# Kernel optimization log

Hardware: AMD Instinct MI355X
Metric: run time of the kernel (lower is better)

Reference implementation:

```python
import jax, jax.numpy as jnp
import numpy as np

B, C, L = 4, 256, 4096
H = 8
DK = C // H


def setup_inputs() -> dict:
    key = jax.random.key(0)
    kx, kq, kk, kv, kl = jax.random.split(key, 5)
    scale = 1.0 / np.sqrt(C)
    return {
        "x": jax.random.normal(kx, (B, C, L), dtype=jnp.float32),
        "Wq": jax.random.normal(kq, (C, C), dtype=jnp.float32) * scale,
        "Wk": jax.random.normal(kk, (C, C), dtype=jnp.float32) * scale,
        "Wv": jax.random.normal(kv, (C, C), dtype=jnp.float32) * scale,
        "Wl": jax.random.normal(kl, (C, C), dtype=jnp.float32) * scale,
    }


def reference(x, Wq, Wk, Wv, Wl):
    # Conv1d with kernel_size=1, no bias == channel-mixing matmul per position.
    def proj(W, t):  # W: [C_out, C_in], t: [B, C_in, L] -> [B, L, H, DK]
        y = jnp.einsum('oc,bcl->blo', W, t)
        return y.reshape(B, L, H, DK)

    q = proj(Wq, x)  # [B, L, H, DK]
    k = proj(Wk, x)
    v = proj(Wv, x)

    # scores: [B, H, L, L]
    scores = jnp.einsum('bqhd,bkhd->bhqk', q, k) / jnp.sqrt(jnp.float32(DK))
    p_attn = jax.nn.softmax(scores, axis=-1)
    # attention output with post-ReLU: [B, L, H, DK] -> [B, L, C]
    out = jax.nn.relu(jnp.einsum('bhqk,bkhd->bqhd', p_attn, v)).reshape(B, L, C)
    # last_conv: [B, C_out, L]
    return jnp.einsum('oc,blc->bol', Wl, out)
```

## Files before the change

### kernel.cpp

```cpp
#include <hip/hip_runtime.h>

#define L_DIM 4096
#define C_DIM 256
#define B_DIM 4
#define NH 8
#define DK 32

#define QSCALE 0.25507694f

typedef __bf16 bf16x8 __attribute__((ext_vector_type(8)));
typedef float  f32x4  __attribute__((ext_vector_type(4)));
typedef float  f32x16 __attribute__((ext_vector_type(16)));

static __device__ __forceinline__ unsigned pk_bf16(float lo, float hi) {
    unsigned a = __builtin_bit_cast(unsigned, lo) + 0x8000u;
    unsigned b = __builtin_bit_cast(unsigned, hi) + 0x8000u;
    return __builtin_amdgcn_perm(b, a, 0x07060302u);
}

__global__ __launch_bounds__(256) void transpose_x_kernel(
    const float* __restrict__ x, __bf16* __restrict__ xt)
{
    const int t  = threadIdx.x;
    const int l0 = blockIdx.x * 64;
    const int c0 = blockIdx.y * 64;
    const int b  = blockIdx.z;

    __shared__ __attribute__((aligned(16))) float T[64][65];

    {
        const int r  = t >> 2;
        const int lc = (t & 3) * 16;
        const float* xp = x + ((size_t)b * C_DIM + c0 + r) * L_DIM + l0 + lc;
        #pragma unroll
        for (int k = 0; k < 4; ++k)
            *(f32x4*)&T[r][lc + k * 4] = *(const f32x4*)(xp + k * 4);
    }
    __syncthreads();
    {
        const int l  = t >> 2;
        const int cc = (t & 3) * 16;
        unsigned u[8];
        #pragma unroll
        for (int i = 0; i < 8; ++i)
            u[i] = pk_bf16(T[cc + 2 * i][l], T[cc + 2 * i + 1][l]);
        __bf16* op = xt + ((size_t)b * L_DIM + l0 + l) * C_DIM + c0 + cc;
        *(uint4*)op       = make_uint4(u[0], u[1], u[2], u[3]);
        *(uint4*)(op + 8) = make_uint4(u[4], u[5], u[6], u[7]);
    }
}

__global__ __launch_bounds__(256) void proj_mfma_kernel(
    const __bf16* __restrict__ xt, const float* __restrict__ Wq,
    const float* __restrict__ Wk, const float* __restrict__ Wv,
    __bf16* __restrict__ Qb, __bf16* __restrict__ Kb, __bf16* __restrict__ Vb)
{
    const int t    = threadIdx.x;
    const int wave = t >> 6;
    const int lane = t & 63;
    const int n32  = lane & 31;
    const int hl   = lane >> 5;
    const int l0   = blockIdx.x * 128;
    const int ob   = blockIdx.y & 1;
    const int p    = blockIdx.y >> 1;
    const int b    = blockIdx.z;
    const float* W = (p == 0) ? Wq : ((p == 1) ? Wk : Wv);
    const float sc = (p == 0) ? QSCALE : 1.0f;

    __shared__ __attribute__((aligned(16))) __bf16 Wt[128][72];
    __shared__ __attribute__((aligned(16))) __bf16 Xs[128][72];

    const int wo  = t >> 1, wcc = (t & 1) * 32;
    const int xl  = t >> 1, xcc = (t & 1) * 32;
    const float*  wg = W + (size_t)(ob * 128 + wo) * C_DIM + wcc;
    const __bf16* xg = xt + ((size_t)b * L_DIM + l0 + xl) * C_DIM + xcc;

    const int moff = (wave & 1) * 64;
    const int noff = (wave >> 1) * 64;

    f32x16 acc[2][2];
    #pragma unroll
    for (int i = 0; i < 2; ++i)
        #pragma unroll
        for (int j = 0; j < 2; ++j)
            #pragma unroll
            for (int r = 0; r < 16; ++r) acc[i][j][r] = 0.f;

    unsigned wpk[16];
    bf16x8   xpr[4];
    #pragma unroll
    for (int k = 0; k < 8; ++k) {
        f32x4 wv = *(const f32x4*)(wg + k * 4);
        wpk[k * 2]     = pk_bf16(wv[0] * sc, wv[1] * sc);
        wpk[k * 2 + 1] = pk_bf16(wv[2] * sc, wv[3] * sc);
    }
    #pragma unroll
    for (int g = 0; g < 4; ++g) xpr[g] = *(const bf16x8*)(xg + g * 8);

    for (int bk = 0; bk < 4; ++bk) {
        __syncthreads();
        #pragma unroll
        for (int g = 0; g < 4; ++g) {
            *(uint4*)&Wt[wo][wcc + g * 8] =
                make_uint4(wpk[g*4], wpk[g*4+1], wpk[g*4+2], wpk[g*4+3]);
            *(bf16x8*)&Xs[xl][xcc + g * 8] = xpr[g];
        }
        if (bk < 3) {
            #pragma unroll
            for (int k = 0; k < 8; ++k) {
                f32x4 wv = *(const f32x4*)(wg + (bk + 1) * 64 + k * 4);
                wpk[k * 2]     = pk_bf16(wv[0] * sc, wv[1] * sc);
                wpk[k * 2 + 1] = pk_bf16(wv[2] * sc, wv[3] * sc);
            }
            #pragma unroll
            for (int g = 0; g < 4; ++g)
                xpr[g] = *(const bf16x8*)(xg + (bk + 1) * 64 + g * 8);
        }
        __syncthreads();

        #pragma unroll
        for (int ks = 0; ks < 4; ++ks) {
            bf16x8 a0 = *(const bf16x8*)&Wt[moff + n32     ][ks * 16 + hl * 8];
            bf16x8 a1 = *(const bf16x8*)&Wt[moff + 32 + n32][ks * 16 + hl * 8];
            bf16x8 b0 = *(const bf16x8*)&Xs[noff + n32     ][ks * 16 + hl * 8];
            bf16x8 b1 = *(const bf16x8*)&Xs[noff + 32 + n32][ks * 16 + hl * 8];
            acc[0][0] = __builtin_amdgcn_mfma_f32_32x32x16_bf16(a0, b0, acc[0][0], 0, 0, 0);
            acc[0][1] = __builtin_amdgcn_mfma_f32_32x32x16_bf16(a0, b1, acc[0][1], 0, 0, 0);
            acc[1][0] = __builtin_amdgcn_mfma_f32_32x32x16_bf16(a1, b0, acc[1][0], 0, 0, 0);
            acc[1][1] = __builtin_amdgcn_mfma_f32_32x32x16_bf16(a1, b1, acc[1][1], 0, 0, 0);
        }
    }

    #pragma unroll
    for (int mt = 0; mt < 2; ++mt) {
        const int o32 = ob * 128 + moff + mt * 32;
        const int h   = o32 >> 5;
        const int bh  = b * NH + h;
        #pragma unroll
        for (int nt = 0; nt < 2; ++nt) {
            const int l = l0 + noff + nt * 32 + n32;
            if (p < 2) {
                __bf16* out = ((p == 0) ? Qb : Kb) + ((size_t)bh * L_DIM + l) * DK;
                #pragma unroll
                for (int g = 0; g < 4; ++g) {
                    unsigned u0 = pk_bf16(acc[mt][nt][g*4],     acc[mt][nt][g*4+1]);
                    unsigned u1 = pk_bf16(acc[mt][nt][g*4+2],   acc[mt][nt][g*4+3]);
                    *(uint2*)(out + 4 * hl + 8 * g) = make_uint2(u0, u1);
                }
            } else {
                #pragma unroll
                for (int r = 0; r < 16; ++r) {
                    const int dk = (r & 3) + 4 * hl + 8 * (r >> 2);
                    Vb[((size_t)bh * DK + dk) * L_DIM + l] = (__bf16)acc[mt][nt][r];
                }
            }
        }
    }
}

__global__ __launch_bounds__(256) void attn_kernel(
    const __bf16* __restrict__ Q, const __bf16* __restrict__ K,
    const __bf16* __restrict__ V, __bf16* __restrict__ Op0,
    __bf16* __restrict__ Op1, float* __restrict__ Ls)
{
    const int tid   = threadIdx.x;
    const int wave  = tid >> 6;
    const int lane  = tid & 63;
    const int n32   = lane & 31;
    const int hl    = lane >> 5;
    const int h     = blockIdx.y;
    const int b     = blockIdx.z >> 1;
    const int khalf = blockIdx.z & 1;
    const int bh    = b * NH + h;
    const int q0    = blockIdx.x * 256 + wave * 64;
    const int kt0   = khalf * 32;

    __shared__ __attribute__((aligned(16))) __bf16 Ks[64][40];
    __shared__ __attribute__((aligned(16))) __bf16 Vs[32][72];

    bf16x8 qf[2][2];
    #pragma unroll
    for (int qt = 0; qt < 2; ++qt) {
        const __bf16* qp = Q + ((size_t)bh * L_DIM + q0 + qt * 32 + n32) * DK;
        qf[qt][0] = *(const bf16x8*)(qp + hl * 8);
        qf[qt][1] = *(const bf16x8*)(qp + 16 + hl * 8);
    }

    f32x16 oacc[2], lacc[2];
    #pragma unroll
    for (int qt = 0; qt < 2; ++qt)
        #pragma unroll
        for (int r = 0; r < 16; ++r) { oacc[qt][r] = 0.f; lacc[qt][r] = 0.f; }

    const f32x16 z16 = {};

    bf16x8 ones;
    #pragma unroll
    for (int j = 0; j < 8; ++j) ones[j] = (__bf16)1.0f;

    const __bf16* kg = K + (size_t)bh * L_DIM * DK + (tid >> 2) * DK + (tid & 3) * 8;
    const __bf16* vg = V + ((size_t)bh * DK + (tid >> 3)) * L_DIM + (tid & 7) * 8;
    __bf16* ksd = &Ks[tid >> 2][(tid & 3) * 8];
    const int va  = tid & 7;
    __bf16* vsd0 = &Vs[tid >> 3][(va >> 1) * 16 + (va & 1) * 4];
    __bf16* vsd1 = vsd0 + 8;

    bf16x8 kreg = *(const bf16x8*)(kg + (size_t)kt0 * 64 * DK);
    bf16x8 vreg = *(const bf16x8*)(vg + kt0 * 64);

    for (int kt = 0; kt < 32; ++kt) {
        __syncthreads();
        *(bf16x8*)ksd = kreg;
        union { bf16x8 v; uint2 u2[2]; } vv; vv.v = vreg;
        *(uint2*)vsd0 = vv.u2[0];
        *(uint2*)vsd1 = vv.u2[1];
        {
            const int nkt = kt0 + ((kt + 1) & 31);
            kreg = *(const bf16x8*)(kg + (size_t)nkt * 64 * DK);
            vreg = *(const bf16x8*)(vg + nkt * 64);
        }
        __syncthreads();

        bf16x8 kf[2][2];
        kf[0][0] = *(const bf16x8*)&Ks[n32     ][hl * 8];
        kf[0][1] = *(const bf16x8*)&Ks[n32     ][16 + hl * 8];
        kf[1][0] = *(const bf16x8*)&Ks[32 + n32][hl * 8];
        kf[1][1] = *(const bf16x8*)&Ks[32 + n32][16 + hl * 8];
        bf16x8 vf[4];
        vf[0] = *(const bf16x8*)&Vs[n32][     hl * 8];
        vf[1] = *(const bf16x8*)&Vs[n32][16 + hl * 8];
        vf[2] = *(const bf16x8*)&Vs[n32][32 + hl * 8];
        vf[3] = *(const bf16x8*)&Vs[n32][48 + hl * 8];

        #pragma unroll
        for (int mt = 0; mt < 2; ++mt) {
            #pragma unroll
            for (int qt = 0; qt < 2; ++qt) {
                f32x16 s = __builtin_amdgcn_mfma_f32_32x32x16_bf16(
                    kf[mt][0], qf[qt][0], z16, 0, 0, 0);
                s = __builtin_amdgcn_mfma_f32_32x32x16_bf16(
                    kf[mt][1], qf[qt][1], s, 0, 0, 0);

                float e[16];
                #pragma unroll
                for (int r = 0; r < 16; ++r) e[r] = __builtin_amdgcn_exp2f(s[r]);
                union { unsigned u[4]; bf16x8 v; } p0, p1;
                #pragma unroll
                for (int i = 0; i < 4; ++i) {
                    p0.u[i] = pk_bf16(e[2 * i],     e[2 * i + 1]);
                    p1.u[i] = pk_bf16(e[8 + 2 * i], e[8 + 2 * i + 1]);
                }

                oacc[qt] = __builtin_amdgcn_mfma_f32_32x32x16_bf16(
                    vf[mt * 2],     p0.v, oacc[qt], 0, 0, 0);
                lacc[qt] = __builtin_amdgcn_mfma_f32_32x32x16_bf16(
                    ones,           p0.v, lacc[qt], 0, 0, 0);
                oacc[qt] = __builtin_amdgcn_mfma_f32_32x32x16_bf16(
                    vf[mt * 2 + 1], p1.v, oacc[qt], 0, 0, 0);
                lacc[qt] = __builtin_amdgcn_mfma_f32_32x32x16_bf16(
                    ones,           p1.v, lacc[qt], 0, 0, 0);
            }
        }
    }

    __bf16* Op = khalf ? Op1 : Op0;
    #pragma unroll
    for (int qt = 0; qt < 2; ++qt) {
        const int l = q0 + qt * 32 + n32;
        __bf16* ap = Op + ((size_t)b * L_DIM + l) * C_DIM + h * 32 + 4 * hl;
        #pragma unroll
        for (int g = 0; g < 4; ++g) {
            *(uint2*)(ap + 8 * g) = make_uint2(
                pk_bf16(oacc[qt][g*4],     oacc[qt][g*4+1]),
                pk_bf16(oacc[qt][g*4+2],   oacc[qt][g*4+3]));
        }
        Ls[((size_t)khalf * B_DIM * NH + bh) * L_DIM + l] = lacc[qt][0];
    }
}

__global__ __launch_bounds__(256) void final_mfma_kernel(
    const __bf16* __restrict__ Op0, const __bf16* __restrict__ Op1,
    const float* __restrict__ Ls, const float* __restrict__ Wl,
    float* __restrict__ y)
{
    const int t    = threadIdx.x;
    const int wave = t >> 6;
    const int lane = t & 63;
    const int n32  = lane & 31;
    const int hl   = lane >> 5;
    const int l0   = blockIdx.x * 64;
    const int ob   = blockIdx.y;
    const int b    = blockIdx.z;

    __shared__ __attribute__((aligned(16))) __bf16 Wt[128][72];
    __shared__ __attribute__((aligned(16))) __bf16 Xs[64][72];

    const int wo  = t >> 1, wcc = (t & 1) * 32;
    const int xl  = t >> 2, xcc = (t & 3) * 16;
    const float* wg = Wl + (size_t)(ob * 128 + wo) * C_DIM + wcc;
    const size_t obase = ((size_t)b * L_DIM + l0 + xl) * C_DIM + xcc;

    float inv[4];
    {
        const int lidx = l0 + xl;
        #pragma unroll
        for (int bk = 0; bk < 4; ++bk) {
            const int hh = (bk * 64 + xcc) >> 5;
            const float l1 = Ls[((size_t)0 * B_DIM * NH + b * NH + hh) * L_DIM + lidx];
            const float l2 = Ls[((size_t)1 * B_DIM * NH + b * NH + hh) * L_DIM + lidx];
            inv[bk] = __builtin_amdgcn_rcpf(l1 + l2);
        }
    }

    const int moff = (wave & 1) * 64;
    const int noff = (wave >> 1) * 32;

    f32x16 acc[2];
    #pragma unroll
    for (int i = 0; i < 2; ++i)
        #pragma unroll
        for (int r = 0; r < 16; ++r) acc[i][r] = 0.f;

    unsigned wpk[16];
    bf16x8   o1r, o2r;
    #pragma unroll
    for (int k = 0; k < 8; ++k) {
        f32x4 wv = *(const f32x4*)(wg + k * 4);
        wpk[k * 2]     = pk_bf16(wv[0], wv[1]);
        wpk[k * 2 + 1] = pk_bf16(wv[2], wv[3]);
    }
    o1r = *(const bf16x8*)(Op0 + obase);
    o2r = *(const bf16x8*)(Op1 + obase);
    bf16x8 o1r2 = *(const bf16x8*)(Op0 + obase + 8);
    bf16x8 o2r2 = *(const bf16x8*)(Op1 + obase + 8);

    for (int bk = 0; bk < 4; ++bk) {
        __syncthreads();
        #pragma unroll
        for (int g = 0; g < 4; ++g)
            *(uint4*)&Wt[wo][wcc + g * 8] =
                make_uint4(wpk[g*4], wpk[g*4+1], wpk[g*4+2], wpk[g*4+3]);
        {
            unsigned u[4];
            #pragma unroll
            for (int i = 0; i < 4; ++i) {
                float v0 = ((float)o1r[2*i]   + (float)o2r[2*i]  ) * inv[bk];
                float v1 = ((float)o1r[2*i+1] + (float)o2r[2*i+1]) * inv[bk];
                v0 = v0 > 0.f ? v0 : 0.f;
                v1 = v1 > 0.f ? v1 : 0.f;
                u[i] = pk_bf16(v0, v1);
            }
            *(uint4*)&Xs[xl][xcc] = make_uint4(u[0], u[1], u[2], u[3]);
            #pragma unroll
            for (int i = 0; i < 4; ++i) {
                float v0 = ((float)o1r2[2*i]   + (float)o2r2[2*i]  ) * inv[bk];
                float v1 = ((float)o1r2[2*i+1] + (float)o2r2[2*i+1]) * inv[bk];
                v0 = v0 > 0.f ? v0 : 0.f;
                v1 = v1 > 0.f ? v1 : 0.f;
                u[i] = pk_bf16(v0, v1);
            }
            *(uint4*)&Xs[xl][xcc + 8] = make_uint4(u[0], u[1], u[2], u[3]);
        }
        if (bk < 3) {
            #pragma unroll
            for (int k = 0; k < 8; ++k) {
                f32x4 wv = *(const f32x4*)(wg + (bk + 1) * 64 + k * 4);
                wpk[k * 2]     = pk_bf16(wv[0], wv[1]);
                wpk[k * 2 + 1] = pk_bf16(wv[2], wv[3]);
            }
            o1r  = *(const bf16x8*)(Op0 + obase + (bk + 1) * 64);
            o2r  = *(const bf16x8*)(Op1 + obase + (bk + 1) * 64);
            o1r2 = *(const bf16x8*)(Op0 + obase + (bk + 1) * 64 + 8);
            o2r2 = *(const bf16x8*)(Op1 + obase + (bk + 1) * 64 + 8);
        }
        __syncthreads();

        #pragma unroll
        for (int ks = 0; ks < 4; ++ks) {
            bf16x8 a0 = *(const bf16x8*)&Wt[moff + n32     ][ks * 16 + hl * 8];
            bf16x8 a1 = *(const bf16x8*)&Wt[moff + 32 + n32][ks * 16 + hl * 8];
            bf16x8 b0 = *(const bf16x8*)&Xs[noff + n32     ][ks * 16 + hl * 8];
            acc[0] = __builtin_amdgcn_mfma_f32_32x32x16_bf16(a0, b0, acc[0], 0, 0, 0);
            acc[1] = __builtin_amdgcn_mfma_f32_32x32x16_bf16(a1, b0, acc[1], 0, 0, 0);
        }
    }

    #pragma unroll
    for (int mt = 0; mt < 2; ++mt) {
        #pragma unroll
        for (int r = 0; r < 16; ++r) {
            const int o = ob * 128 + moff + mt * 32 + (r & 3) + 4 * hl + 8 * (r >> 2);
            y[((size_t)b * C_DIM + o) * L_DIM + l0 + noff + n32] = acc[mt][r];
        }
    }
}

extern "C" void kernel_launch(void* const* d_in, const int* in_sizes, int n_in,
                              void* d_out, int out_size, void* d_ws, size_t ws_size,
                              hipStream_t stream)
{
    const float* x  = (const float*)d_in[0];
    const float* Wq = (const float*)d_in[1];
    const float* Wk = (const float*)d_in[2];
    const float* Wv = (const float*)d_in[3];
    const float* Wl = (const float*)d_in[4];
    float* y = (float*)d_out;

    const size_t n = (size_t)B_DIM * NH * L_DIM * DK;
    __bf16* Qb  = (__bf16*)d_ws;
    __bf16* Kb  = Qb + n;
    __bf16* Vb  = Kb + n;
    __bf16* Xt  = Vb + n;
    __bf16* Op0 = Xt;
    __bf16* Op1 = Xt + n;
    float*  Ls  = (float*)(Op1 + n);

    transpose_x_kernel<<<dim3(L_DIM/64, C_DIM/64, B_DIM), 256, 0, stream>>>(x, Xt);
    proj_mfma_kernel<<<dim3(L_DIM/128, 6, B_DIM), 256, 0, stream>>>(
        Xt, Wq, Wk, Wv, Qb, Kb, Vb);
    attn_kernel<<<dim3(L_DIM/256, NH, B_DIM * 2), 256, 0, stream>>>(
        Qb, Kb, Vb, Op0, Op1, Ls);
    final_mfma_kernel<<<dim3(L_DIM/64, 2, B_DIM), 256, 0, stream>>>(
        Op0, Op1, Ls, Wl, y);
}
```

Baseline: 216.3 us.

## Overlap global prefetch with MFMA compute and compute softmax denominator on VALU

```diff
diff --git a/kernel.cpp b/kernel.cpp
--- a/kernel.cpp
+++ b/kernel.cpp
@@ -86,14 +86,10 @@
             #pragma unroll
             for (int r = 0; r < 16; ++r) acc[i][j][r] = 0.f;
 
-    unsigned wpk[16];
-    bf16x8   xpr[4];
-    #pragma unroll
-    for (int k = 0; k < 8; ++k) {
-        f32x4 wv = *(const f32x4*)(wg + k * 4);
-        wpk[k * 2]     = pk_bf16(wv[0] * sc, wv[1] * sc);
-        wpk[k * 2 + 1] = pk_bf16(wv[2] * sc, wv[3] * sc);
-    }
+    f32x4  wraw[8];
+    bf16x8 xpr[4];
+    #pragma unroll
+    for (int k = 0; k < 8; ++k) wraw[k] = *(const f32x4*)(wg + k * 4);
     #pragma unroll
     for (int g = 0; g < 4; ++g) xpr[g] = *(const bf16x8*)(xg + g * 8);
 
@@ -101,22 +97,24 @@
         __syncthreads();
         #pragma unroll
         for (int g = 0; g < 4; ++g) {
-            *(uint4*)&Wt[wo][wcc + g * 8] =
-                make_uint4(wpk[g*4], wpk[g*4+1], wpk[g*4+2], wpk[g*4+3]);
+            unsigned u0 = pk_bf16(wraw[g*2][0] * sc, wraw[g*2][1] * sc);
+            unsigned u1 = pk_bf16(wraw[g*2][2] * sc, wraw[g*2][3] * sc);
+            unsigned u2 = pk_bf16(wraw[g*2+1][0] * sc, wraw[g*2+1][1] * sc);
+            unsigned u3 = pk_bf16(wraw[g*2+1][2] * sc, wraw[g*2+1][3] * sc);
+            *(uint4*)&Wt[wo][wcc + g * 8] = make_uint4(u0, u1, u2, u3);
             *(bf16x8*)&Xs[xl][xcc + g * 8] = xpr[g];
         }
-        if (bk < 3) {
-            #pragma unroll
-            for (int k = 0; k < 8; ++k) {
-                f32x4 wv = *(const f32x4*)(wg + (bk + 1) * 64 + k * 4);
-                wpk[k * 2]     = pk_bf16(wv[0] * sc, wv[1] * sc);
-                wpk[k * 2 + 1] = pk_bf16(wv[2] * sc, wv[3] * sc);
-            }
+        __syncthreads();
+
+        {
+            const int nbk = (bk + 1) & 3;
+            #pragma unroll
+            for (int k = 0; k < 8; ++k)
+                wraw[k] = *(const f32x4*)(wg + nbk * 64 + k * 4);
             #pragma unroll
             for (int g = 0; g < 4; ++g)
-                xpr[g] = *(const bf16x8*)(xg + (bk + 1) * 64 + g * 8);
-        }
-        __syncthreads();
+                xpr[g] = *(const bf16x8*)(xg + nbk * 64 + g * 8);
+        }
 
         #pragma unroll
         for (int ks = 0; ks < 4; ++ks) {
@@ -186,17 +184,14 @@
         qf[qt][1] = *(const bf16x8*)(qp + 16 + hl * 8);
     }
 
-    f32x16 oacc[2], lacc[2];
+    f32x16 oacc[2];
+    float  lsum[2] = {0.f, 0.f};
     #pragma unroll
     for (int qt = 0; qt < 2; ++qt)
         #pragma unroll
-        for (int r = 0; r < 16; ++r) { oacc[qt][r] = 0.f; lacc[qt][r] = 0.f; }
+        for (int r = 0; r < 16; ++r) oacc[qt][r] = 0.f;
 
     const f32x16 z16 = {};
-
-    bf16x8 ones;
-    #pragma unroll
-    for (int j = 0; j < 8; ++j) ones[j] = (__bf16)1.0f;
 
     const __bf16* kg = K + (size_t)bh * L_DIM * DK + (tid >> 2) * DK + (tid & 3) * 8;
     const __bf16* vg = V + ((size_t)bh * DK + (tid >> 3)) * L_DIM + (tid & 7) * 8;
@@ -214,12 +209,13 @@
         union { bf16x8 v; uint2 u2[2]; } vv; vv.v = vreg;
         *(uint2*)vsd0 = vv.u2[0];
         *(uint2*)vsd1 = vv.u2[1];
+        __syncthreads();
+
         {
             const int nkt = kt0 + ((kt + 1) & 31);
             kreg = *(const bf16x8*)(kg + (size_t)nkt * 64 * DK);
             vreg = *(const bf16x8*)(vg + nkt * 64);
         }
-        __syncthreads();
 
         bf16x8 kf[2][2];
         kf[0][0] = *(const bf16x8*)&Ks[n32     ][hl * 8];
@@ -250,15 +246,13 @@
                     p0.u[i] = pk_bf16(e[2 * i],     e[2 * i + 1]);
                     p1.u[i] = pk_bf16(e[8 + 2 * i], e[8 + 2 * i + 1]);
                 }
+                lsum[qt] += (((e[0]+e[1])+(e[2]+e[3]))+((e[4]+e[5])+(e[6]+e[7])))
+                          + (((e[8]+e[9])+(e[10]+e[11]))+((e[12]+e[13])+(e[14]+e[15])));
 
                 oacc[qt] = __builtin_amdgcn_mfma_f32_32x32x16_bf16(
                     vf[mt * 2],     p0.v, oacc[qt], 0, 0, 0);
-                lacc[qt] = __builtin_amdgcn_mfma_f32_32x32x16_bf16(
-                    ones,           p0.v, lacc[qt], 0, 0, 0);
                 oacc[qt] = __builtin_amdgcn_mfma_f32_32x32x16_bf16(
                     vf[mt * 2 + 1], p1.v, oacc[qt], 0, 0, 0);
-                lacc[qt] = __builtin_amdgcn_mfma_f32_32x32x16_bf16(
-                    ones,           p1.v, lacc[qt], 0, 0, 0);
             }
         }
     }
@@ -266,6 +260,7 @@
     __bf16* Op = khalf ? Op1 : Op0;
     #pragma unroll
     for (int qt = 0; qt < 2; ++qt) {
+        const float ltot = lsum[qt] + __shfl_xor(lsum[qt], 32);
         const int l = q0 + qt * 32 + n32;
         __bf16* ap = Op + ((size_t)b * L_DIM + l) * C_DIM + h * 32 + 4 * hl;
         #pragma unroll
@@ -274,7 +269,7 @@
                 pk_bf16(oacc[qt][g*4],     oacc[qt][g*4+1]),
                 pk_bf16(oacc[qt][g*4+2],   oacc[qt][g*4+3]));
         }
-        Ls[((size_t)khalf * B_DIM * NH + bh) * L_DIM + l] = lacc[qt][0];
+        Ls[((size_t)khalf * B_DIM * NH + bh) * L_DIM + l] = ltot;
     }
 }
 
@@ -321,25 +316,25 @@
         #pragma unroll
         for (int r = 0; r < 16; ++r) acc[i][r] = 0.f;
 
-    unsigned wpk[16];
-    bf16x8   o1r, o2r;
-    #pragma unroll
-    for (int k = 0; k < 8; ++k) {
-        f32x4 wv = *(const f32x4*)(wg + k * 4);
-        wpk[k * 2]     = pk_bf16(wv[0], wv[1]);
-        wpk[k * 2 + 1] = pk_bf16(wv[2], wv[3]);
-    }
-    o1r = *(const bf16x8*)(Op0 + obase);
-    o2r = *(const bf16x8*)(Op1 + obase);
-    bf16x8 o1r2 = *(const bf16x8*)(Op0 + obase + 8);
-    bf16x8 o2r2 = *(const bf16x8*)(Op1 + obase + 8);
+    f32x4  wraw[8];
+    bf16x8 o1r, o2r, o1r2, o2r2;
+    #pragma unroll
+    for (int k = 0; k < 8; ++k) wraw[k] = *(const f32x4*)(wg + k * 4);
+    o1r  = *(const bf16x8*)(Op0 + obase);
+    o2r  = *(const bf16x8*)(Op1 + obase);
+    o1r2 = *(const bf16x8*)(Op0 + obase + 8);
+    o2r2 = *(const bf16x8*)(Op1 + obase + 8);
 
     for (int bk = 0; bk < 4; ++bk) {
         __syncthreads();
         #pragma unroll
-        for (int g = 0; g < 4; ++g)
-            *(uint4*)&Wt[wo][wcc + g * 8] =
-                make_uint4(wpk[g*4], wpk[g*4+1], wpk[g*4+2], wpk[g*4+3]);
+        for (int g = 0; g < 4; ++g) {
+            unsigned u0 = pk_bf16(wraw[g*2][0], wraw[g*2][1]);
+            unsigned u1 = pk_bf16(wraw[g*2][2], wraw[g*2][3]);
+            unsigned u2 = pk_bf16(wraw[g*2+1][0], wraw[g*2+1][1]);
+            unsigned u3 = pk_bf16(wraw[g*2+1][2], wraw[g*2+1][3]);
+            *(uint4*)&Wt[wo][wcc + g * 8] = make_uint4(u0, u1, u2, u3);
+        }
         {
             unsigned u[4];
             #pragma unroll
@@ -361,19 +356,18 @@
             }
             *(uint4*)&Xs[xl][xcc + 8] = make_uint4(u[0], u[1], u[2], u[3]);
         }
-        if (bk < 3) {
-            #pragma unroll
-            for (int k = 0; k < 8; ++k) {
-                f32x4 wv = *(const f32x4*)(wg + (bk + 1) * 64 + k * 4);
-                wpk[k * 2]     = pk_bf16(wv[0], wv[1]);
-                wpk[k * 2 + 1] = pk_bf16(wv[2], wv[3]);
-            }
-            o1r  = *(const bf16x8*)(Op0 + obase + (bk + 1) * 64);
-            o2r  = *(const bf16x8*)(Op1 + obase + (bk + 1) * 64);
-            o1r2 = *(const bf16x8*)(Op0 + obase + (bk + 1) * 64 + 8);
-            o2r2 = *(const bf16x8*)(Op1 + obase + (bk + 1) * 64 + 8);
-        }
-        __syncthreads();
+        __syncthreads();
+
+        {
+            const int nbk = (bk + 1) & 3;
+            #pragma unroll
+            for (int k = 0; k < 8; ++k)
+                wraw[k] = *(const f32x4*)(wg + nbk * 64 + k * 4);
+            o1r  = *(const bf16x8*)(Op0 + obase + nbk * 64);
+            o2r  = *(const bf16x8*)(Op1 + obase + nbk * 64);
+            o1r2 = *(const bf16x8*)(Op0 + obase + nbk * 64 + 8);
+            o2r2 = *(const bf16x8*)(Op1 + obase + nbk * 64 + 8);
+        }
 
         #pragma unroll
         for (int ks = 0; ks < 4; ++ks) {
```

Result: slower. 230.6 us (+6.6%).
